# Kernel tuning notes

Hardware: AMD Instinct MI355X
Metric: run time of the kernel (lower is better)

## Reference

```python
import jax, jax.numpy as jnp
import numpy as np

EPS = 1e-06
ALPHA = 0.5
SIGMA = 50.0
INF = 1e12  # 'infinity' for empty cells; INF + L^2 stays representable in fp32


def _dt_last(f):
    """Exact 1D squared Euclidean distance transform along the last axis:
    out[..., i] = min_j f[..., j] + (i - j)^2  (min-plus with parabola kernel).
    Scanned over output index i to avoid materializing an [..., L, L] tensor."""
    L = f.shape[-1]
    idx = jnp.arange(L)

    def step(carry, i):
        row = jnp.min(f + ((i - idx) ** 2).astype(f.dtype), axis=-1)
        return carry, row

    _, out = jax.lax.scan(step, None, idx)  # [L, ...batch]
    return jnp.moveaxis(out, 0, -1)


def _edt(mask):
    """Euclidean distance from every pixel to the nearest True pixel, per sample.
    mask: [B, H, W] bool. Equivalent to scipy.ndimage.distance_transform_edt(~mask)."""
    f = jnp.where(mask, jnp.float32(0.0), jnp.float32(INF))
    f = jnp.swapaxes(_dt_last(jnp.swapaxes(f, 1, 2)), 1, 2)  # pass along H
    f = _dt_last(f)                                          # pass along W
    return jnp.sqrt(f)


def _weight_map(targets):
    mask = targets > 0
    dist = _edt(mask)
    w = 1.0 - jnp.exp(-dist / SIGMA)
    has_fg = jnp.any(mask, axis=(1, 2))  # torch code leaves weight 0 for empty masks
    return jnp.where(has_fg[:, None, None], w, jnp.float32(0.0))


def setup_inputs() -> dict:
    key = jax.random.key(0)
    k1, k2 = jax.random.split(key)
    B, H, W = 16, 512, 512
    logits = jax.random.normal(k1, (B, H, W), dtype=jnp.float32)
    targets = (jax.random.uniform(k2, (B, H, W)) < 0.01).astype(jnp.float32)
    return {"logits": logits, "targets": targets}


def reference(logits, targets):
    probs = jax.nn.sigmoid(logits)
    inter = jnp.sum(probs * targets)
    union = jnp.sum(probs) + jnp.sum(targets) - inter
    soft_iou_loss = 1.0 - (inter + EPS) / (union + EPS)
    weight = _weight_map(targets)
    distance_penalty = jnp.mean(weight * probs * (1.0 - targets))
    return soft_iou_loss + ALPHA * distance_penalty
```

## Files before the change

kernel.cpp:

```cpp
#include <hip/hip_runtime.h>
#include <math.h>

#define BB 16
#define HH 512
#define WW 512
#define NPIX (BB*HH*WW)
#define NWORDS 16
#define HB 256
#define HWORDS 8
#define NBLK 1024

__device__ inline unsigned int even16(unsigned int x) {
  x &= 0x55555555u;
  x = (x | (x >> 1)) & 0x33333333u;
  x = (x | (x >> 2)) & 0x0F0F0F0Fu;
  x = (x | (x >> 4)) & 0x00FF00FFu;
  x = (x | (x >> 8)) & 0x0000FFFFu;
  return x;
}

__global__ __launch_bounds__(256) void build_kernel(
    const float* __restrict__ tg, unsigned int* __restrict__ mask,
    unsigned int* __restrict__ hmask, short* __restrict__ un_h,
    short* __restrict__ dn_h) {
  __shared__ unsigned int smask[NWORDS][32];
  __shared__ unsigned int hsm[HWORDS][16];
  int wt = blockIdx.x & 15;
  int b  = blockIdx.x >> 4;
  int c2 = threadIdx.x & 15;
  int k  = threadIdx.x >> 4;
  int w  = (wt << 5) + (c2 << 1);
  const float* p = tg + ((size_t)(b * HH + (k << 5))) * WW + w;
  unsigned int w0 = 0, w1 = 0;
  #pragma unroll
  for (int r = 0; r < 32; ++r) {
    float2 v = *(const float2*)&p[(size_t)r * WW];
    w0 |= (v.x > 0.f ? 1u : 0u) << r;
    w1 |= (v.y > 0.f ? 1u : 0u) << r;
  }
  smask[k][(c2 << 1)] = w0;
  smask[k][(c2 << 1) + 1] = w1;
  *(uint2*)&mask[(b * NWORDS + k) * WW + w] = make_uint2(w0, w1);
  __syncthreads();
  int t = threadIdx.x;
  if (t < 128) {
    int kp  = t >> 4;
    int bcl = t & 15;
    unsigned int wa = smask[2 * kp][2 * bcl] | smask[2 * kp][2 * bcl + 1];
    unsigned int wb = smask[2 * kp + 1][2 * bcl] | smask[2 * kp + 1][2 * bcl + 1];
    unsigned int hword = even16(wa | (wa >> 1)) | (even16(wb | (wb >> 1)) << 16);
    hsm[kp][bcl] = hword;
    hmask[(b * HWORDS + kp) * HB + (wt << 4) + bcl] = hword;
  }
  __syncthreads();
  if (t < 16) {
    int bc = (wt << 4) + t;
    int cur = 16000;
    un_h[(b * 9 + 8) * HB + bc] = (short)cur;
    #pragma unroll
    for (int kp = HWORDS - 1; kp >= 0; --kp) {
      unsigned int m = hsm[kp][t];
      if (m) cur = (kp << 5) + (int)__builtin_ctz(m);
      un_h[(b * 9 + kp) * HB + bc] = (short)cur;
    }
  } else if (t >= 64 && t < 80) {
    int tt = t - 64;
    int bc = (wt << 4) + tt;
    int cur = -16000;
    dn_h[(b * 9 + 0) * HB + bc] = (short)cur;
    #pragma unroll
    for (int kp = 0; kp < HWORDS; ++kp) {
      unsigned int m = hsm[kp][tt];
      if (m) cur = (kp << 5) + 31 - (int)__builtin_clz(m);
      dn_h[(b * 9 + kp + 1) * HB + bc] = (short)cur;
    }
  }
}

__global__ __launch_bounds__(256) void edt_loss_kernel(
    const float* __restrict__ logits, const unsigned int* __restrict__ mask,
    const unsigned int* __restrict__ hmask, const short* __restrict__ un_h,
    const short* __restrict__ dn_h, float* __restrict__ partials) {
  __shared__ __align__(16) float srow[4][768];
  __shared__ float wsum[4][4];

  int g = blockIdx.x;
  int b = g >> 6, Rbase = (g & 63) << 2;
  int tid = threadIdx.x;
  int wv = tid >> 6, lane = tid & 63;
  int R = Rbase + wv;
  int c0 = lane << 2;
  float* sA = &srow[wv][256];

  *(float4*)&srow[wv][lane << 2] = make_float4(3e12f, 3e12f, 3e12f, 3e12f);
  *(float4*)&srow[wv][512 + (lane << 2)] = make_float4(3e12f, 3e12f, 3e12f, 3e12f);

  int k0 = R >> 5, pos = R & 31;
  unsigned int pmask_lo = (1u << pos) - 1u;
  unsigned int pmask_le = pmask_lo | (1u << pos);
  int kb = k0 << 5;
  uint4 hm = *(const uint4*)&hmask[(b * HWORDS + k0) * HB + c0];
  short4 un4 = *(const short4*)&un_h[(b * 9 + k0 + 1) * HB + c0];
  short4 dn4 = *(const short4*)&dn_h[(b * 9 + k0) * HB + c0];

  float dv0, dv1, dv2, dv3;
#define VERT(MC, UNC, DNC, DVOUT)                                         \
  { unsigned int upm  = (MC) & ~pmask_lo;                                 \
    unsigned int lowm = (MC) & pmask_le;                                  \
    int up  = upm  ? (kb + (int)__builtin_ctz(upm))        : (int)(UNC);  \
    int dnv = lowm ? (kb + 31 - (int)__builtin_clz(lowm))  : (int)(DNC);  \
    int bv = min(up - R, R - dnv);                                        \
    DVOUT = (bv > 255) ? 1e12f : (float)(bv * bv); }
  VERT(hm.x, un4.x, dn4.x, dv0)
  VERT(hm.y, un4.y, dn4.y, dv1)
  VERT(hm.z, un4.z, dn4.z, dv2)
  VERT(hm.w, un4.w, dn4.w, dv3)
#undef VERT
  *(float4*)&sA[c0] = make_float4(dv0, dv1, dv2, dv3);
  __syncthreads();

  float b0 = dv0, b1 = dv1, b2 = dv2, b3 = dv3;
  for (int o0 = 1; o0 < HB; o0 += 8) {
    float bmax = fmaxf(fmaxf(b0, b1), fmaxf(b2, b3));
    if (__all((float)(o0 * o0) >= bmax)) break;
    const float2* Lp = (const float2*)&sA[c0 - o0 - 7];
    const float2* Rp = (const float2*)&sA[c0 + o0 - 1];
    float2 L0 = Lp[0], L1 = Lp[1], L2 = Lp[2], L3 = Lp[3], L4 = Lp[4], L5 = Lp[5];
    float2 R0 = Rp[0], R1 = Rp[1], R2 = Rp[2], R3 = Rp[3], R4 = Rp[4], R5 = Rp[5];
#define STEP(U, A0, B0, A1, B1, A2, B2, A3, B3)             \
    { float oo = (float)((o0 + (U)) * (o0 + (U)));          \
      b0 = fminf(b0, fminf((A0), (B0)) + oo);               \
      b1 = fminf(b1, fminf((A1), (B1)) + oo);               \
      b2 = fminf(b2, fminf((A2), (B2)) + oo);               \
      b3 = fminf(b3, fminf((A3), (B3)) + oo); }
    STEP(0, L3.y, R0.y, L4.x, R1.x, L4.y, R1.y, L5.x, R2.x)
    STEP(1, L3.x, R1.x, L3.y, R1.y, L4.x, R2.x, L4.y, R2.y)
    STEP(2, L2.y, R1.y, L3.x, R2.x, L3.y, R2.y, L4.x, R3.x)
    STEP(3, L2.x, R2.x, L2.y, R2.y, L3.x, R3.x, L3.y, R3.y)
    STEP(4, L1.y, R2.y, L2.x, R3.x, L2.y, R3.y, L3.x, R4.x)
    STEP(5, L1.x, R3.x, L1.y, R3.y, L2.x, R4.x, L2.y, R4.y)
    STEP(6, L0.y, R3.y, L1.x, R4.x, L1.y, R4.y, L2.x, R5.x)
    STEP(7, L0.x, R4.x, L0.y, R4.y, L1.x, R5.x, L1.y, R5.y)
#undef STEP
  }

#define WGT(BC) (((BC) > 1e9f) ? 0.f \
                 : (1.f - __expf(-__builtin_amdgcn_sqrtf(BC) * 0.04f)))
  float wg0 = WGT(b0), wg1 = WGT(b1), wg2 = WGT(b2), wg3 = WGT(b3);
#undef WGT

  float acc_p = 0.f, acc_t = 0.f, acc_pt = 0.f, acc_pen = 0.f;
  int wcl = lane << 3;
#define PX(XC, WC, MC, BIT)                                 \
  { float x = (XC);                                         \
    float tt = (float)(((MC) >> (BIT)) & 1u);               \
    float e = __expf(-x);                                   \
    float pp = __builtin_amdgcn_rcpf(1.f + e);              \
    acc_p += pp; acc_t += tt; acc_pt += pp * tt;            \
    acc_pen += (WC) * pp * (1.f - tt); }
#define ROW_LOSS(RR)                                                        \
  { int i = (R << 1) + (RR);                                                \
    int bit = i & 31;                                                       \
    size_t lb = ((size_t)(b * HH + i)) * WW + wcl;                          \
    const unsigned int* mrow = &mask[(b * NWORDS + (i >> 5)) * WW + wcl];   \
    float4 xA = *(const float4*)&logits[lb];                                \
    float4 xB = *(const float4*)&logits[lb + 4];                            \
    uint4 mA = *(const uint4*)&mrow[0];                                     \
    uint4 mB = *(const uint4*)&mrow[4];                                     \
    PX(xA.x, wg0, mA.x, bit) PX(xA.y, wg0, mA.y, bit)                       \
    PX(xA.z, wg1, mA.z, bit) PX(xA.w, wg1, mA.w, bit)                       \
    PX(xB.x, wg2, mB.x, bit) PX(xB.y, wg2, mB.y, bit)                       \
    PX(xB.z, wg3, mB.z, bit) PX(xB.w, wg3, mB.w, bit) }
  ROW_LOSS(0)
  ROW_LOSS(1)
#undef ROW_LOSS
#undef PX

  #pragma unroll
  for (int off = 32; off; off >>= 1) {
    acc_p  += __shfl_down(acc_p,  off);
    acc_t  += __shfl_down(acc_t,  off);
    acc_pt += __shfl_down(acc_pt, off);
    acc_pen += __shfl_down(acc_pen, off);
  }
  if (lane == 0) {
    wsum[wv][0] = acc_p; wsum[wv][1] = acc_t;
    wsum[wv][2] = acc_pt; wsum[wv][3] = acc_pen;
  }
  __syncthreads();
  if (tid == 0) {
    float r0 = 0.f, r1 = 0.f, r2 = 0.f, r3 = 0.f;
    #pragma unroll
    for (int q = 0; q < 4; ++q) {
      r0 += wsum[q][0]; r1 += wsum[q][1];
      r2 += wsum[q][2]; r3 += wsum[q][3];
    }
    partials[0 * NBLK + g] = r0;
    partials[1 * NBLK + g] = r1;
    partials[2 * NBLK + g] = r2;
    partials[3 * NBLK + g] = r3;
  }
}

__global__ __launch_bounds__(256) void finalize_kernel(
    const float* __restrict__ partials, float* __restrict__ out) {
  __shared__ float wsum[4][4];
  int tid = threadIdx.x;
  float a0 = 0.f, a1 = 0.f, a2 = 0.f, a3 = 0.f;
  for (int k = tid; k < NBLK; k += 256) {
    a0 += partials[0 * NBLK + k];
    a1 += partials[1 * NBLK + k];
    a2 += partials[2 * NBLK + k];
    a3 += partials[3 * NBLK + k];
  }
  #pragma unroll
  for (int off = 32; off; off >>= 1) {
    a0 += __shfl_down(a0, off);
    a1 += __shfl_down(a1, off);
    a2 += __shfl_down(a2, off);
    a3 += __shfl_down(a3, off);
  }
  int wave = tid >> 6, lane = tid & 63;
  if (lane == 0) {
    wsum[wave][0] = a0; wsum[wave][1] = a1;
    wsum[wave][2] = a2; wsum[wave][3] = a3;
  }
  __syncthreads();
  if (tid == 0) {
    float sp = 0.f, st = 0.f, inter = 0.f, pen = 0.f;
    #pragma unroll
    for (int wv = 0; wv < 4; ++wv) {
      sp += wsum[wv][0]; st += wsum[wv][1];
      inter += wsum[wv][2]; pen += wsum[wv][3];
    }
    float uni = sp + st - inter;
    float iou_loss = 1.f - (inter + 1e-6f) / (uni + 1e-6f);
    float penalty = pen / (float)NPIX;
    out[0] = iou_loss + 0.5f * penalty;
  }
}

extern "C" void kernel_launch(void* const* d_in, const int* in_sizes, int n_in,
                              void* d_out, int out_size, void* d_ws, size_t ws_size,
                              hipStream_t stream) {
  const float* logits = (const float*)d_in[0];
  const float* tg     = (const float*)d_in[1];
  char* base = (char*)d_ws;
  unsigned int* mask  = (unsigned int*)base;
  unsigned int* hmask = (unsigned int*)(base + 524288);
  short* un_h = (short*)(base + 655360);
  short* dn_h = (short*)(base + 729088);
  float* partials = (float*)(base + 802816);
  float* out = (float*)d_out;

  hipLaunchKernelGGL(build_kernel, dim3(256), dim3(256), 0, stream,
                     tg, mask, hmask, un_h, dn_h);
  hipLaunchKernelGGL(edt_loss_kernel, dim3(NBLK), dim3(256), 0, stream,
                     logits, mask, hmask, un_h, dn_h, partials);
  hipLaunchKernelGGL(finalize_kernel, dim3(1), dim3(256), 0, stream,
                     partials, out);
}
```

Before: 19.44 us.

## Fuse finalize into loss kernel via last-block atomic counter and prefetch logits

Removes the separate finalize kernel launch: each block publishes its partial sums with agent-scope atomics, bumps a two-level counter (32 sub-counters plus a master), and the last block to finish reduces all partials and writes the output. Counters are zeroed in the build kernel. Separately, the logits loads are hoisted to the start of the loss kernel so their latency overlaps with the EDT computation. This saves one launch and its gap, at the cost of atomic traffic, relaxed-ordering correctness risk, and extra live registers for the prefetched values.

```diff
diff --git a/kernel.cpp b/kernel.cpp
--- a/kernel.cpp
+++ b/kernel.cpp
@@ -22,7 +22,7 @@
 __global__ __launch_bounds__(256) void build_kernel(
     const float* __restrict__ tg, unsigned int* __restrict__ mask,
     unsigned int* __restrict__ hmask, short* __restrict__ un_h,
-    short* __restrict__ dn_h) {
+    short* __restrict__ dn_h, unsigned int* __restrict__ counters) {
   __shared__ unsigned int smask[NWORDS][32];
   __shared__ unsigned int hsm[HWORDS][16];
   int wt = blockIdx.x & 15;
@@ -30,6 +30,7 @@
   int c2 = threadIdx.x & 15;
   int k  = threadIdx.x >> 4;
   int w  = (wt << 5) + (c2 << 1);
+  if (blockIdx.x == 0 && threadIdx.x < 33) counters[threadIdx.x] = 0u;
   const float* p = tg + ((size_t)(b * HH + (k << 5))) * WW + w;
   unsigned int w0 = 0, w1 = 0;
   #pragma unroll
@@ -80,9 +81,11 @@
 __global__ __launch_bounds__(256) void edt_loss_kernel(
     const float* __restrict__ logits, const unsigned int* __restrict__ mask,
     const unsigned int* __restrict__ hmask, const short* __restrict__ un_h,
-    const short* __restrict__ dn_h, float* __restrict__ partials) {
+    const short* __restrict__ dn_h, float* __restrict__ partials,
+    unsigned int* __restrict__ counters, float* __restrict__ out) {
   __shared__ __align__(16) float srow[4][768];
   __shared__ float wsum[4][4];
+  __shared__ int lastflag;
 
   int g = blockIdx.x;
   int b = g >> 6, Rbase = (g & 63) << 2;
@@ -94,6 +97,13 @@
 
   *(float4*)&srow[wv][lane << 2] = make_float4(3e12f, 3e12f, 3e12f, 3e12f);
   *(float4*)&srow[wv][512 + (lane << 2)] = make_float4(3e12f, 3e12f, 3e12f, 3e12f);
+
+  int wcl = lane << 3;
+  size_t lb0 = ((size_t)(b * HH + (R << 1))) * WW + wcl;
+  float4 xA0 = *(const float4*)&logits[lb0];
+  float4 xB0 = *(const float4*)&logits[lb0 + 4];
+  float4 xA1 = *(const float4*)&logits[lb0 + WW];
+  float4 xB1 = *(const float4*)&logits[lb0 + WW + 4];
 
   int k0 = R >> 5, pos = R & 31;
   unsigned int pmask_lo = (1u << pos) - 1u;
@@ -150,7 +160,6 @@
 #undef WGT
 
   float acc_p = 0.f, acc_t = 0.f, acc_pt = 0.f, acc_pen = 0.f;
-  int wcl = lane << 3;
 #define PX(XC, WC, MC, BIT)                                 \
   { float x = (XC);                                         \
     float tt = (float)(((MC) >> (BIT)) & 1u);               \
@@ -158,21 +167,18 @@
     float pp = __builtin_amdgcn_rcpf(1.f + e);              \
     acc_p += pp; acc_t += tt; acc_pt += pp * tt;            \
     acc_pen += (WC) * pp * (1.f - tt); }
-#define ROW_LOSS(RR)                                                        \
+#define ROW_LOSS(RR, XA, XB)                                                \
   { int i = (R << 1) + (RR);                                                \
     int bit = i & 31;                                                       \
-    size_t lb = ((size_t)(b * HH + i)) * WW + wcl;                          \
     const unsigned int* mrow = &mask[(b * NWORDS + (i >> 5)) * WW + wcl];   \
-    float4 xA = *(const float4*)&logits[lb];                                \
-    float4 xB = *(const float4*)&logits[lb + 4];                            \
     uint4 mA = *(const uint4*)&mrow[0];                                     \
     uint4 mB = *(const uint4*)&mrow[4];                                     \
-    PX(xA.x, wg0, mA.x, bit) PX(xA.y, wg0, mA.y, bit)                       \
-    PX(xA.z, wg1, mA.z, bit) PX(xA.w, wg1, mA.w, bit)                       \
-    PX(xB.x, wg2, mB.x, bit) PX(xB.y, wg2, mB.y, bit)                       \
-    PX(xB.z, wg3, mB.z, bit) PX(xB.w, wg3, mB.w, bit) }
-  ROW_LOSS(0)
-  ROW_LOSS(1)
+    PX(XA.x, wg0, mA.x, bit) PX(XA.y, wg0, mA.y, bit)                       \
+    PX(XA.z, wg1, mA.z, bit) PX(XA.w, wg1, mA.w, bit)                       \
+    PX(XB.x, wg2, mB.x, bit) PX(XB.y, wg2, mB.y, bit)                       \
+    PX(XB.z, wg3, mB.z, bit) PX(XB.w, wg3, mB.w, bit) }
+  ROW_LOSS(0, xA0, xB0)
+  ROW_LOSS(1, xA1, xB1)
 #undef ROW_LOSS
 #undef PX
 
@@ -195,48 +201,65 @@
       r0 += wsum[q][0]; r1 += wsum[q][1];
       r2 += wsum[q][2]; r3 += wsum[q][3];
     }
-    partials[0 * NBLK + g] = r0;
-    partials[1 * NBLK + g] = r1;
-    partials[2 * NBLK + g] = r2;
-    partials[3 * NBLK + g] = r3;
-  }
-}
-
-__global__ __launch_bounds__(256) void finalize_kernel(
-    const float* __restrict__ partials, float* __restrict__ out) {
-  __shared__ float wsum[4][4];
-  int tid = threadIdx.x;
-  float a0 = 0.f, a1 = 0.f, a2 = 0.f, a3 = 0.f;
-  for (int k = tid; k < NBLK; k += 256) {
-    a0 += partials[0 * NBLK + k];
-    a1 += partials[1 * NBLK + k];
-    a2 += partials[2 * NBLK + k];
-    a3 += partials[3 * NBLK + k];
-  }
-  #pragma unroll
-  for (int off = 32; off; off >>= 1) {
-    a0 += __shfl_down(a0, off);
-    a1 += __shfl_down(a1, off);
-    a2 += __shfl_down(a2, off);
-    a3 += __shfl_down(a3, off);
-  }
-  int wave = tid >> 6, lane = tid & 63;
-  if (lane == 0) {
-    wsum[wave][0] = a0; wsum[wave][1] = a1;
-    wsum[wave][2] = a2; wsum[wave][3] = a3;
-  }
-  __syncthreads();
-  if (tid == 0) {
-    float sp = 0.f, st = 0.f, inter = 0.f, pen = 0.f;
-    #pragma unroll
-    for (int wv = 0; wv < 4; ++wv) {
-      sp += wsum[wv][0]; st += wsum[wv][1];
-      inter += wsum[wv][2]; pen += wsum[wv][3];
-    }
-    float uni = sp + st - inter;
-    float iou_loss = 1.f - (inter + 1e-6f) / (uni + 1e-6f);
-    float penalty = pen / (float)NPIX;
-    out[0] = iou_loss + 0.5f * penalty;
+    __hip_atomic_store(&partials[0 * NBLK + g], r0, __ATOMIC_RELAXED,
+                       __HIP_MEMORY_SCOPE_AGENT);
+    __hip_atomic_store(&partials[1 * NBLK + g], r1, __ATOMIC_RELAXED,
+                       __HIP_MEMORY_SCOPE_AGENT);
+    __hip_atomic_store(&partials[2 * NBLK + g], r2, __ATOMIC_RELAXED,
+                       __HIP_MEMORY_SCOPE_AGENT);
+    __hip_atomic_store(&partials[3 * NBLK + g], r3, __ATOMIC_RELAXED,
+                       __HIP_MEMORY_SCOPE_AGENT);
+    asm volatile("s_waitcnt vmcnt(0)" ::: "memory");
+    unsigned int sub = __hip_atomic_fetch_add(&counters[g & 31], 1u,
+                                              __ATOMIC_RELAXED,
+                                              __HIP_MEMORY_SCOPE_AGENT);
+    int last = 0;
+    if (sub == 31u) {
+      unsigned int mst = __hip_atomic_fetch_add(&counters[32], 1u,
+                                                __ATOMIC_RELAXED,
+                                                __HIP_MEMORY_SCOPE_AGENT);
+      last = (mst == 31u) ? 1 : 0;
+    }
+    lastflag = last;
+  }
+  __syncthreads();
+
+  if (lastflag) {
+    float a0 = 0.f, a1 = 0.f, a2 = 0.f, a3 = 0.f;
+    for (int kq = tid; kq < NBLK; kq += 256) {
+      a0 += __hip_atomic_load(&partials[0 * NBLK + kq], __ATOMIC_RELAXED,
+                              __HIP_MEMORY_SCOPE_AGENT);
+      a1 += __hip_atomic_load(&partials[1 * NBLK + kq], __ATOMIC_RELAXED,
+                              __HIP_MEMORY_SCOPE_AGENT);
+      a2 += __hip_atomic_load(&partials[2 * NBLK + kq], __ATOMIC_RELAXED,
+                              __HIP_MEMORY_SCOPE_AGENT);
+      a3 += __hip_atomic_load(&partials[3 * NBLK + kq], __ATOMIC_RELAXED,
+                              __HIP_MEMORY_SCOPE_AGENT);
+    }
+    #pragma unroll
+    for (int off = 32; off; off >>= 1) {
+      a0 += __shfl_down(a0, off);
+      a1 += __shfl_down(a1, off);
+      a2 += __shfl_down(a2, off);
+      a3 += __shfl_down(a3, off);
+    }
+    if (lane == 0) {
+      wsum[wv][0] = a0; wsum[wv][1] = a1;
+      wsum[wv][2] = a2; wsum[wv][3] = a3;
+    }
+    __syncthreads();
+    if (tid == 0) {
+      float sp = 0.f, st = 0.f, inter = 0.f, pen = 0.f;
+      #pragma unroll
+      for (int q = 0; q < 4; ++q) {
+        sp += wsum[q][0]; st += wsum[q][1];
+        inter += wsum[q][2]; pen += wsum[q][3];
+      }
+      float uni = sp + st - inter;
+      float iou_loss = 1.f - (inter + 1e-6f) / (uni + 1e-6f);
+      float penalty = pen / (float)NPIX;
+      out[0] = iou_loss + 0.5f * penalty;
+    }
   }
 }
 
@@ -251,12 +274,11 @@
   short* un_h = (short*)(base + 655360);
   short* dn_h = (short*)(base + 729088);
   float* partials = (float*)(base + 802816);
+  unsigned int* counters = (unsigned int*)(base + 819200);
   float* out = (float*)d_out;
 
   hipLaunchKernelGGL(build_kernel, dim3(256), dim3(256), 0, stream,
-                     tg, mask, hmask, un_h, dn_h);
+                     tg, mask, hmask, un_h, dn_h, counters);
   hipLaunchKernelGGL(edt_loss_kernel, dim3(NBLK), dim3(256), 0, stream,
-                     logits, mask, hmask, un_h, dn_h, partials);
-  hipLaunchKernelGGL(finalize_kernel, dim3(1), dim3(256), 0, stream,
-                     partials, out);
-}
+                     logits, mask, hmask, un_h, dn_h, partials, counters, out);
+}
```

Result: slower. 22.80 us (+17.3%).
